# Kernel optimization log

Hardware: AMD Instinct MI355X
Metric: run time of the kernel (lower is better)

Reference implementation:

```python
import jax, jax.numpy as jnp
import numpy as np

N_NODES = 50000
N_EDGES = 800000
IN_DIM = 128
HIDDEN = 64
HEADS = 4
OUT_DIM = 32
NEG_SLOPE = 0.2  # PyG GATConv default negative_slope


def _glorot(key, shape):
    fan = shape[0] + shape[-1]
    return jax.random.normal(key, shape, dtype=jnp.float32) * jnp.sqrt(2.0 / fan)


def setup_inputs() -> dict:
    key = jax.random.key(0)
    ks = jax.random.split(key, 8)
    x = jax.random.normal(ks[0], (N_NODES, IN_DIM), dtype=jnp.float32)
    edge_index = jax.random.randint(ks[1], (2, N_EDGES), 0, N_NODES, dtype=jnp.int64)
    return {
        "x": x,
        "edge_index": edge_index,
        "W1": _glorot(ks[2], (IN_DIM, HEADS * HIDDEN)),
        "a_src1": _glorot(ks[3], (HEADS, HIDDEN)),
        "a_dst1": _glorot(ks[4], (HEADS, HIDDEN)),
        "b1": jnp.zeros((HEADS * HIDDEN,), dtype=jnp.float32),
        "W2": _glorot(ks[5], (HEADS * HIDDEN, OUT_DIM)),
        "a_src2": _glorot(ks[6], (1, OUT_DIM)),
        "a_dst2": _glorot(ks[7], (1, OUT_DIM)),
        "b2": jnp.zeros((OUT_DIM,), dtype=jnp.float32),
    }


def gat_conv(x, src, dst, W, a_src, a_dst, b, heads, feat, concat):
    """PyG-style GATConv (self-loops already appended to src/dst)."""
    n = x.shape[0]
    h = (x @ W).reshape(n, heads, feat)              # [N, H, F]
    alpha_s = jnp.einsum("nhf,hf->nh", h, a_src)     # [N, H]
    alpha_d = jnp.einsum("nhf,hf->nh", h, a_dst)     # [N, H]
    logits = jax.nn.leaky_relu(alpha_s[src] + alpha_d[dst], NEG_SLOPE)  # [E, H]
    # segment softmax over edges grouped by destination node
    seg_max = jax.ops.segment_max(logits, dst, num_segments=n)          # [N, H]
    expd = jnp.exp(logits - seg_max[dst])
    seg_sum = jax.ops.segment_sum(expd, dst, num_segments=n)            # [N, H]
    alpha = expd / (seg_sum[dst] + 1e-16)                               # [E, H]
    # scatter-aggregate weighted messages from source nodes
    out = jax.ops.segment_sum(h[src] * alpha[:, :, None], dst, num_segments=n)  # [N, H, F]
    out = out.reshape(n, heads * feat) if concat else out.mean(axis=1)
    return out + b


def reference(x, edge_index, W1, a_src1, a_dst1, b1, W2, a_src2, a_dst2, b2):
    n = x.shape[0]
    loop = jnp.arange(n, dtype=edge_index.dtype)
    src = jnp.concatenate([edge_index[0], loop])  # add_self_loops=True (PyG default)
    dst = jnp.concatenate([edge_index[1], loop])
    h = jax.nn.elu(gat_conv(x, src, dst, W1, a_src1, a_dst1, b1, HEADS, HIDDEN, True))
    return gat_conv(h, src, dst, W2, a_src2, a_dst2, b2, 1, OUT_DIM, False)
```

## Files before the change

kernel.cpp:

```cpp
#include <hip/hip_runtime.h>
#include <hip/hip_bf16.h>

#define N_NODES 50000
#define N_EDGES 800000
#define E_TOT   850000
#define IN_DIM  128
#define C1      256
#define HEADS   4
#define HID     64
#define OUT_DIM 32
#define NEG_SLOPE 0.2f
#define SCAN_NBLK 196

typedef __attribute__((ext_vector_type(8))) short bf16x8;
typedef __attribute__((ext_vector_type(8))) unsigned short u16x8;
typedef __attribute__((ext_vector_type(4))) float f32x4;

__device__ __forceinline__ void edge_sd(const int* __restrict__ ei, int e, int& s, int& d) {
    if (e < N_EDGES) { s = ei[e]; d = ei[N_EDGES + e]; }
    else             { s = d = e - N_EDGES; }
}

__device__ __forceinline__ unsigned short f2bf(float f) {
    unsigned u = __float_as_uint(f);
    u += 0x7fffu + ((u >> 16) & 1u);
    return (unsigned short)(u >> 16);
}
__device__ __forceinline__ float bf2f(unsigned short u) {
    return __uint_as_float(((unsigned)u) << 16);
}
__device__ __forceinline__ float4 bf4_to_f4(ushort4 v) {
    return make_float4(bf2f(v.x), bf2f(v.y), bf2f(v.z), bf2f(v.w));
}

__global__ __launch_bounds__(256) void setup_kernel(const float* __restrict__ W1,
                                                    const float* __restrict__ W2,
                                                    unsigned short* __restrict__ Bp1,
                                                    unsigned short* __restrict__ Bp2,
                                                    int* __restrict__ degcur) {
    int tid = blockIdx.x * 256 + threadIdx.x;
    if (tid < 2 * N_NODES) degcur[tid] = 0;
    if (tid < IN_DIM * C1) {
        int j = tid & 7, q = (tid >> 3) & 3, n = (tid >> 5) & 255, K0 = tid >> 13;
        int k = K0 * 32 + q * 8 + j;
        Bp1[tid] = f2bf(W1[k * C1 + n]);
        if (tid < C1 * OUT_DIM) {
            int j2 = tid & 7, q2 = (tid >> 3) & 3, n2 = (tid >> 5) & 31, K02 = tid >> 10;
            int k2 = K02 * 32 + q2 * 8 + j2;
            Bp2[tid] = f2bf(W2[k2 * OUT_DIM + n2]);
        }
    }
}

__global__ __launch_bounds__(256) void deg_kernel(const int* __restrict__ ei,
                                                  int* __restrict__ deg) {
    int e = blockIdx.x * 256 + threadIdx.x;
    if (e >= E_TOT) return;
    int s, d; edge_sd(ei, e, s, d);
    atomicAdd(&deg[d], 1);
}

__global__ __launch_bounds__(256) void scanA_kernel(const int* __restrict__ deg,
                                                    int* __restrict__ incl,
                                                    int* __restrict__ blocksum) {
    __shared__ int sm[256];
    int t = threadIdx.x, idx = blockIdx.x * 256 + t;
    int v = (idx < N_NODES) ? deg[idx] : 0;
    sm[t] = v; __syncthreads();
#pragma unroll
    for (int off = 1; off < 256; off <<= 1) {
        int u = (t >= off) ? sm[t - off] : 0;
        __syncthreads();
        sm[t] += u;
        __syncthreads();
    }
    if (idx < N_NODES) incl[idx] = sm[t];
    if (t == 255) blocksum[blockIdx.x] = sm[t];
}

__global__ __launch_bounds__(256) void scanC_kernel(const int* __restrict__ deg,
                                                    const int* __restrict__ incl,
                                                    const int* __restrict__ blocksum,
                                                    int* __restrict__ row_start) {
    __shared__ int wsum[4];
    int t = threadIdx.x;
    int v = (t < (int)blockIdx.x) ? blocksum[t] : 0;
#pragma unroll
    for (int m = 32; m >= 1; m >>= 1) v += __shfl_xor(v, m, 64);
    if ((t & 63) == 0) wsum[t >> 6] = v;
    __syncthreads();
    int off = wsum[0] + wsum[1] + wsum[2] + wsum[3];
    int idx = blockIdx.x * 256 + t;
    if (idx >= N_NODES) return;
    row_start[idx] = off + incl[idx] - deg[idx];
    if (idx == N_NODES - 1) row_start[N_NODES] = off + incl[idx];
}

__global__ __launch_bounds__(256) void scatter_kernel(const int* __restrict__ ei,
                                                      const int* __restrict__ row_start,
                                                      int* __restrict__ cursor,
                                                      int* __restrict__ csr_src) {
    int e = blockIdx.x * 256 + threadIdx.x;
    if (e >= E_TOT) return;
    int s, d; edge_sd(ei, e, s, d);
    int pos = atomicAdd(&cursor[d], 1);
    csr_src[row_start[d] + pos] = s;
}

__global__ __launch_bounds__(256) void gemm1_kernel(const float* __restrict__ x,
                                                    const unsigned short* __restrict__ Bp,
                                                    const float* __restrict__ a_src1,
                                                    const float* __restrict__ a_dst1,
                                                    unsigned short* __restrict__ h1b,
                                                    float* __restrict__ as1,
                                                    float* __restrict__ ad1) {
    __shared__ unsigned short xs[16][136];
    const int t = threadIdx.x;
    const int row0 = blockIdx.x * 16;
    {
        int r = t >> 4, k0 = (t & 15) * 8;
        const float* xp = &x[(size_t)(row0 + r) * IN_DIM + k0];
        float4 v0 = *(const float4*)xp;
        float4 v1 = *(const float4*)(xp + 4);
        ushort4 o0, o1;
        o0.x = f2bf(v0.x); o0.y = f2bf(v0.y); o0.z = f2bf(v0.z); o0.w = f2bf(v0.w);
        o1.x = f2bf(v1.x); o1.y = f2bf(v1.y); o1.z = f2bf(v1.z); o1.w = f2bf(v1.w);
        *(ushort4*)&xs[r][k0] = o0;
        *(ushort4*)&xs[r][k0 + 4] = o1;
    }
    __syncthreads();
    const int wave = t >> 6;
    const int lane = t & 63;
    const int nl = lane & 15, q = lane >> 4;
    f32x4 acc[4];
    f32x4 z = {0.f, 0.f, 0.f, 0.f};
    acc[0] = z; acc[1] = z; acc[2] = z; acc[3] = z;
#pragma unroll
    for (int K0 = 0; K0 < 4; ++K0) {
        bf16x8 af = *(const bf16x8*)&xs[nl][K0 * 32 + q * 8];
#pragma unroll
        for (int sub = 0; sub < 4; ++sub) {
            int n = wave * 64 + sub * 16 + nl;
            bf16x8 bfv = *(const bf16x8*)&Bp[((size_t)(K0 * 256 + n) * 4 + q) * 8];
            acc[sub] = __builtin_amdgcn_mfma_f32_16x16x32_bf16(af, bfv, acc[sub], 0, 0, 0);
        }
    }
    float asv[4], adv[4];
#pragma unroll
    for (int sub = 0; sub < 4; ++sub) {
        asv[sub] = a_src1[wave * 64 + sub * 16 + nl];
        adv[sub] = a_dst1[wave * 64 + sub * 16 + nl];
    }
#pragma unroll
    for (int r = 0; r < 4; ++r) {
        int gr = row0 + q * 4 + r;
        float ps = 0.f, pd = 0.f;
#pragma unroll
        for (int sub = 0; sub < 4; ++sub) {
            float v = acc[sub][r];
            h1b[(size_t)gr * C1 + wave * 64 + sub * 16 + nl] = f2bf(v);
            ps += v * asv[sub];
            pd += v * adv[sub];
        }
#pragma unroll
        for (int m = 8; m >= 1; m >>= 1) {
            ps += __shfl_xor(ps, m, 16);
            pd += __shfl_xor(pd, m, 16);
        }
        if (nl == 0) {
            as1[gr * 4 + wave] = ps;
            ad1[gr * 4 + wave] = pd;
        }
    }
}

__global__ __launch_bounds__(256) void agg1_kernel(const int* __restrict__ csr_src,
                                                   const int* __restrict__ row_start,
                                                   const unsigned short* __restrict__ h1b,
                                                   const float* __restrict__ as1,
                                                   const float* __restrict__ ad1,
                                                   const float* __restrict__ b1,
                                                   unsigned short* __restrict__ hpb) {
    int n = (blockIdx.x * 256 + threadIdx.x) >> 6;
    if (n >= N_NODES) return;
    int lane = threadIdx.x & 63;
    int h = lane >> 4;
    int beg = row_start[n], end = row_start[n + 1];
    float ad = ad1[n * 4 + h];
    float4 acc = make_float4(0.f, 0.f, 0.f, 0.f);
    float sumw = 0.f;
    int i = beg;
    for (; i + 8 <= end; i += 8) {
        int s[8];
#pragma unroll
        for (int u = 0; u < 8; ++u) s[u] = csr_src[i + u];
        ushort4 rv[8];
#pragma unroll
        for (int u = 0; u < 8; ++u) rv[u] = *(const ushort4*)&h1b[(size_t)s[u] * C1 + lane * 4];
        float a[8];
#pragma unroll
        for (int u = 0; u < 8; ++u) a[u] = as1[s[u] * 4 + h];
#pragma unroll
        for (int u = 0; u < 8; ++u) {
            float l = a[u] + ad;
            l = l > 0.f ? l : NEG_SLOPE * l;
            float w = __expf(l);
            sumw += w;
            float4 f = bf4_to_f4(rv[u]);
            acc.x += w * f.x; acc.y += w * f.y; acc.z += w * f.z; acc.w += w * f.w;
        }
    }
    if (i < end) {
        int s[8]; bool va[8];
#pragma unroll
        for (int u = 0; u < 8; ++u) {
            va[u] = (i + u) < end;
            s[u] = csr_src[va[u] ? i + u : beg];
        }
        ushort4 rv[8];
#pragma unroll
        for (int u = 0; u < 8; ++u) rv[u] = *(const ushort4*)&h1b[(size_t)s[u] * C1 + lane * 4];
        float a[8];
#pragma unroll
        for (int u = 0; u < 8; ++u) a[u] = as1[s[u] * 4 + h];
#pragma unroll
        for (int u = 0; u < 8; ++u) {
            float l = a[u] + ad;
            l = l > 0.f ? l : NEG_SLOPE * l;
            float w = va[u] ? __expf(l) : 0.f;
            sumw += w;
            float4 f = bf4_to_f4(rv[u]);
            acc.x += w * f.x; acc.y += w * f.y; acc.z += w * f.z; acc.w += w * f.w;
        }
    }
    float inv = 1.f / (sumw + 1e-16f);
    const float4 bv = *(const float4*)&b1[lane * 4];
    float v0 = acc.x * inv + bv.x;
    float v1 = acc.y * inv + bv.y;
    float v2 = acc.z * inv + bv.z;
    float v3 = acc.w * inv + bv.w;
    v0 = v0 > 0.f ? v0 : __expf(v0) - 1.f;
    v1 = v1 > 0.f ? v1 : __expf(v1) - 1.f;
    v2 = v2 > 0.f ? v2 : __expf(v2) - 1.f;
    v3 = v3 > 0.f ? v3 : __expf(v3) - 1.f;
    ushort4 o;
    o.x = f2bf(v0); o.y = f2bf(v1); o.z = f2bf(v2); o.w = f2bf(v3);
    *(ushort4*)&hpb[(size_t)n * C1 + lane * 4] = o;
}

__global__ __launch_bounds__(256) void gemm2_kernel(const unsigned short* __restrict__ hpb,
                                                    const unsigned short* __restrict__ Bp2,
                                                    const float* __restrict__ a_src2,
                                                    const float* __restrict__ a_dst2,
                                                    unsigned short* __restrict__ h2b,
                                                    float* __restrict__ as2,
                                                    float* __restrict__ ad2) {
    __shared__ unsigned short xs[64][264];
    const int t = threadIdx.x;
    const int row0 = blockIdx.x * 64;
    for (int idx = t; idx < 2048; idx += 256) {
        int r = idx >> 5, ch = (idx & 31) * 8;
        int gr = row0 + r;
        u16x8 v = {0, 0, 0, 0, 0, 0, 0, 0};
        if (gr < N_NODES) v = *(const u16x8*)&hpb[(size_t)gr * C1 + ch];
        *(u16x8*)&xs[r][ch] = v;
    }
    __syncthreads();
    const int wave = t >> 6, lane = t & 63;
    const int nl = lane & 15, q = lane >> 4;
    f32x4 acc0 = {0.f, 0.f, 0.f, 0.f}, acc1 = {0.f, 0.f, 0.f, 0.f};
#pragma unroll
    for (int K0 = 0; K0 < 8; ++K0) {
        bf16x8 af = *(const bf16x8*)&xs[wave * 16 + nl][K0 * 32 + q * 8];
        bf16x8 b0 = *(const bf16x8*)&Bp2[((size_t)(K0 * 32 + nl) * 4 + q) * 8];
        bf16x8 b1v = *(const bf16x8*)&Bp2[((size_t)(K0 * 32 + 16 + nl) * 4 + q) * 8];
        acc0 = __builtin_amdgcn_mfma_f32_16x16x32_bf16(af, b0, acc0, 0, 0, 0);
        acc1 = __builtin_amdgcn_mfma_f32_16x16x32_bf16(af, b1v, acc1, 0, 0, 0);
    }
    float a_s0 = a_src2[nl], a_s1 = a_src2[16 + nl];
    float a_d0 = a_dst2[nl], a_d1 = a_dst2[16 + nl];
#pragma unroll
    for (int r = 0; r < 4; ++r) {
        int gr = row0 + wave * 16 + q * 4 + r;
        if (gr < N_NODES) {
            h2b[(size_t)gr * OUT_DIM + nl] = f2bf(acc0[r]);
            h2b[(size_t)gr * OUT_DIM + 16 + nl] = f2bf(acc1[r]);
            float ps = acc0[r] * a_s0 + acc1[r] * a_s1;
            float pd = acc0[r] * a_d0 + acc1[r] * a_d1;
#pragma unroll
            for (int m = 8; m >= 1; m >>= 1) {
                ps += __shfl_xor(ps, m, 16);
                pd += __shfl_xor(pd, m, 16);
            }
            if (nl == 0) { as2[gr] = ps; ad2[gr] = pd; }
        }
    }
}

__global__ __launch_bounds__(256) void agg2_kernel(const int* __restrict__ csr_src,
                                                   const int* __restrict__ row_start,
                                                   const unsigned short* __restrict__ h2b,
                                                   const float* __restrict__ as2,
                                                   const float* __restrict__ ad2,
                                                   const float* __restrict__ b2,
                                                   float* __restrict__ out) {
    int n = (blockIdx.x * 256 + threadIdx.x) >> 6;
    if (n >= N_NODES) return;
    int lane = threadIdx.x & 63;
    int g  = lane >> 3;
    int c4 = lane & 7;
    int beg = row_start[n], end = row_start[n + 1];
    float ad = ad2[n];
    float4 acc = make_float4(0.f, 0.f, 0.f, 0.f);
    float sumw = 0.f;
    for (int i = beg; i < end; i += 8) {
        int idx = i + g;
        bool valid = idx < end;
        int ic = valid ? idx : beg;
        int s = csr_src[ic];
        float l = as2[s] + ad;
        l = l > 0.f ? l : NEG_SLOPE * l;
        float w = valid ? __expf(l) : 0.f;
        sumw += w;
        float4 hv = bf4_to_f4(*(const ushort4*)&h2b[(size_t)s * OUT_DIM + c4 * 4]);
        acc.x += w * hv.x; acc.y += w * hv.y; acc.z += w * hv.z; acc.w += w * hv.w;
    }
#pragma unroll
    for (int m = 8; m <= 32; m <<= 1) {
        sumw  += __shfl_xor(sumw, m, 64);
        acc.x += __shfl_xor(acc.x, m, 64);
        acc.y += __shfl_xor(acc.y, m, 64);
        acc.z += __shfl_xor(acc.z, m, 64);
        acc.w += __shfl_xor(acc.w, m, 64);
    }
    if (g == 0) {
        float inv = 1.f / (sumw + 1e-16f);
        const float4 bv = *(const float4*)&b2[c4 * 4];
        *(float4*)&out[(size_t)n * OUT_DIM + c4 * 4] =
            make_float4(acc.x * inv + bv.x, acc.y * inv + bv.y,
                        acc.z * inv + bv.z, acc.w * inv + bv.w);
    }
}

extern "C" void kernel_launch(void* const* d_in, const int* in_sizes, int n_in,
                              void* d_out, int out_size, void* d_ws, size_t ws_size,
                              hipStream_t stream) {
    const float* x      = (const float*)d_in[0];
    const int*   ei     = (const int*)d_in[1];
    const float* W1     = (const float*)d_in[2];
    const float* a_src1 = (const float*)d_in[3];
    const float* a_dst1 = (const float*)d_in[4];
    const float* b1     = (const float*)d_in[5];
    const float* W2     = (const float*)d_in[6];
    const float* a_src2 = (const float*)d_in[7];
    const float* a_dst2 = (const float*)d_in[8];
    const float* b2     = (const float*)d_in[9];
    float* out = (float*)d_out;

    unsigned short* h1b = (unsigned short*)d_ws;
    unsigned short* hpb = h1b + 12800000;
    unsigned short* h2b = hpb + 12800000;
    unsigned short* Bp1 = h2b + 1600000;
    unsigned short* Bp2 = Bp1 + 32768;
    float* as1    = (float*)(Bp2 + 8192);
    float* ad1    = as1 + 200000;
    float* as2    = ad1 + 200000;
    float* ad2    = as2 + 50000;
    int* csr_src  = (int*)(ad2 + 50000);
    int* row_start= csr_src + E_TOT;
    int* deg      = row_start + (N_NODES + 1);
    int* cursor   = deg + N_NODES;
    int* incl     = cursor + N_NODES;
    int* blocksum = incl + N_NODES;

    const int EB = (E_TOT + 255) / 256;
    setup_kernel<<<391, 256, 0, stream>>>(W1, W2, Bp1, Bp2, deg);
    deg_kernel<<<EB, 256, 0, stream>>>(ei, deg);
    scanA_kernel<<<SCAN_NBLK, 256, 0, stream>>>(deg, incl, blocksum);
    scanC_kernel<<<SCAN_NBLK, 256, 0, stream>>>(deg, incl, blocksum, row_start);
    scatter_kernel<<<EB, 256, 0, stream>>>(ei, row_start, cursor, csr_src);

    gemm1_kernel<<<N_NODES / 16, 256, 0, stream>>>(x, Bp1, a_src1, a_dst1, h1b, as1, ad1);
    agg1_kernel<<<(N_NODES * 64 + 255) / 256, 256, 0, stream>>>(csr_src, row_start, h1b, as1, ad1, b1, hpb);

    gemm2_kernel<<<(N_NODES + 63) / 64, 256, 0, stream>>>(hpb, Bp2, a_src2, a_dst2, h2b, as2, ad2);
    agg2_kernel<<<(N_NODES * 64 + 255) / 256, 256, 0, stream>>>(csr_src, row_start, h2b, as2, ad2, b2, out);
}
```

Baseline: 302.9 us.

## Record atomic slot in degree pass and precompute CSR-ordered edge weights

The degree kernel now stores each edge's atomic slot, so the scatter pass places edges without a second atomic. Scatter now runs after gemm1 and also computes exp(leaky_relu(as+ad)) for all four heads per edge. It writes these weights in CSR order into a new buffer. agg1 reads the precomputed weights contiguously instead of gathering as1 and recomputing the exp in every lane. Row bounds and source indices are made wave-uniform with readfirstlane. The cost is an extra per-edge weight buffer and position array, roughly 17 MB more memory traffic.

```diff
diff --git a/kernel.cpp b/kernel.cpp
--- a/kernel.cpp
+++ b/kernel.cpp
@@ -37,9 +37,9 @@
                                                     const float* __restrict__ W2,
                                                     unsigned short* __restrict__ Bp1,
                                                     unsigned short* __restrict__ Bp2,
-                                                    int* __restrict__ degcur) {
+                                                    int* __restrict__ deg) {
     int tid = blockIdx.x * 256 + threadIdx.x;
-    if (tid < 2 * N_NODES) degcur[tid] = 0;
+    if (tid < N_NODES) deg[tid] = 0;
     if (tid < IN_DIM * C1) {
         int j = tid & 7, q = (tid >> 3) & 3, n = (tid >> 5) & 255, K0 = tid >> 13;
         int k = K0 * 32 + q * 8 + j;
@@ -53,11 +53,12 @@
 }
 
 __global__ __launch_bounds__(256) void deg_kernel(const int* __restrict__ ei,
-                                                  int* __restrict__ deg) {
+                                                  int* __restrict__ deg,
+                                                  int* __restrict__ pos) {
     int e = blockIdx.x * 256 + threadIdx.x;
     if (e >= E_TOT) return;
     int s, d; edge_sd(ei, e, s, d);
-    atomicAdd(&deg[d], 1);
+    pos[e] = atomicAdd(&deg[d], 1);
 }
 
 __global__ __launch_bounds__(256) void scanA_kernel(const int* __restrict__ deg,
@@ -96,15 +97,27 @@
     if (idx == N_NODES - 1) row_start[N_NODES] = off + incl[idx];
 }
 
-__global__ __launch_bounds__(256) void scatter_kernel(const int* __restrict__ ei,
-                                                      const int* __restrict__ row_start,
-                                                      int* __restrict__ cursor,
-                                                      int* __restrict__ csr_src) {
+__global__ __launch_bounds__(256) void scatter_w_kernel(const int* __restrict__ ei,
+                                                        const int* __restrict__ row_start,
+                                                        const int* __restrict__ pos,
+                                                        const float* __restrict__ as1,
+                                                        const float* __restrict__ ad1,
+                                                        int* __restrict__ csr_src,
+                                                        float* __restrict__ wc) {
     int e = blockIdx.x * 256 + threadIdx.x;
     if (e >= E_TOT) return;
     int s, d; edge_sd(ei, e, s, d);
-    int pos = atomicAdd(&cursor[d], 1);
-    csr_src[row_start[d] + pos] = s;
+    int p = row_start[d] + pos[e];
+    csr_src[p] = s;
+    float4 av = *(const float4*)&as1[s * 4];
+    float4 bv = *(const float4*)&ad1[d * 4];
+    float l0 = av.x + bv.x, l1 = av.y + bv.y, l2 = av.z + bv.z, l3 = av.w + bv.w;
+    l0 = l0 > 0.f ? l0 : NEG_SLOPE * l0;
+    l1 = l1 > 0.f ? l1 : NEG_SLOPE * l1;
+    l2 = l2 > 0.f ? l2 : NEG_SLOPE * l2;
+    l3 = l3 > 0.f ? l3 : NEG_SLOPE * l3;
+    *(float4*)&wc[(size_t)p * 4] =
+        make_float4(__expf(l0), __expf(l1), __expf(l2), __expf(l3));
 }
 
 __global__ __launch_bounds__(256) void gemm1_kernel(const float* __restrict__ x,
@@ -177,60 +190,56 @@
 __global__ __launch_bounds__(256) void agg1_kernel(const int* __restrict__ csr_src,
                                                    const int* __restrict__ row_start,
                                                    const unsigned short* __restrict__ h1b,
-                                                   const float* __restrict__ as1,
-                                                   const float* __restrict__ ad1,
+                                                   const float* __restrict__ wc,
                                                    const float* __restrict__ b1,
                                                    unsigned short* __restrict__ hpb) {
     int n = (blockIdx.x * 256 + threadIdx.x) >> 6;
     if (n >= N_NODES) return;
     int lane = threadIdx.x & 63;
     int h = lane >> 4;
-    int beg = row_start[n], end = row_start[n + 1];
-    float ad = ad1[n * 4 + h];
+    int beg = __builtin_amdgcn_readfirstlane(row_start[n]);
+    int end = __builtin_amdgcn_readfirstlane(row_start[n + 1]);
     float4 acc = make_float4(0.f, 0.f, 0.f, 0.f);
     float sumw = 0.f;
     int i = beg;
     for (; i + 8 <= end; i += 8) {
         int s[8];
 #pragma unroll
-        for (int u = 0; u < 8; ++u) s[u] = csr_src[i + u];
+        for (int u = 0; u < 8; ++u) s[u] = __builtin_amdgcn_readfirstlane(csr_src[i + u]);
+        float w[8];
+#pragma unroll
+        for (int u = 0; u < 8; ++u) w[u] = wc[(size_t)(i + u) * 4 + h];
         ushort4 rv[8];
 #pragma unroll
         for (int u = 0; u < 8; ++u) rv[u] = *(const ushort4*)&h1b[(size_t)s[u] * C1 + lane * 4];
-        float a[8];
-#pragma unroll
-        for (int u = 0; u < 8; ++u) a[u] = as1[s[u] * 4 + h];
 #pragma unroll
         for (int u = 0; u < 8; ++u) {
-            float l = a[u] + ad;
-            l = l > 0.f ? l : NEG_SLOPE * l;
-            float w = __expf(l);
-            sumw += w;
+            sumw += w[u];
             float4 f = bf4_to_f4(rv[u]);
-            acc.x += w * f.x; acc.y += w * f.y; acc.z += w * f.z; acc.w += w * f.w;
+            acc.x += w[u] * f.x; acc.y += w[u] * f.y;
+            acc.z += w[u] * f.z; acc.w += w[u] * f.w;
         }
     }
     if (i < end) {
-        int s[8]; bool va[8];
+        int s[8]; int ic[8]; bool va[8];
 #pragma unroll
         for (int u = 0; u < 8; ++u) {
             va[u] = (i + u) < end;
-            s[u] = csr_src[va[u] ? i + u : beg];
-        }
+            ic[u] = va[u] ? i + u : beg;
+            s[u] = __builtin_amdgcn_readfirstlane(csr_src[ic[u]]);
+        }
+        float w[8];
+#pragma unroll
+        for (int u = 0; u < 8; ++u) w[u] = va[u] ? wc[(size_t)ic[u] * 4 + h] : 0.f;
         ushort4 rv[8];
 #pragma unroll
         for (int u = 0; u < 8; ++u) rv[u] = *(const ushort4*)&h1b[(size_t)s[u] * C1 + lane * 4];
-        float a[8];
-#pragma unroll
-        for (int u = 0; u < 8; ++u) a[u] = as1[s[u] * 4 + h];
 #pragma unroll
         for (int u = 0; u < 8; ++u) {
-            float l = a[u] + ad;
-            l = l > 0.f ? l : NEG_SLOPE * l;
-            float w = va[u] ? __expf(l) : 0.f;
-            sumw += w;
+            sumw += w[u];
             float4 f = bf4_to_f4(rv[u]);
-            acc.x += w * f.x; acc.y += w * f.y; acc.z += w * f.z; acc.w += w * f.w;
+            acc.x += w[u] * f.x; acc.y += w[u] * f.y;
+            acc.z += w[u] * f.z; acc.w += w[u] * f.w;
         }
     }
     float inv = 1.f / (sumw + 1e-16f);
@@ -309,7 +318,8 @@
     int lane = threadIdx.x & 63;
     int g  = lane >> 3;
     int c4 = lane & 7;
-    int beg = row_start[n], end = row_start[n + 1];
+    int beg = __builtin_amdgcn_readfirstlane(row_start[n]);
+    int end = __builtin_amdgcn_readfirstlane(row_start[n + 1]);
     float ad = ad2[n];
     float4 acc = make_float4(0.f, 0.f, 0.f, 0.f);
     float sumw = 0.f;
@@ -366,22 +376,23 @@
     float* ad1    = as1 + 200000;
     float* as2    = ad1 + 200000;
     float* ad2    = as2 + 50000;
-    int* csr_src  = (int*)(ad2 + 50000);
+    float* wc     = ad2 + 50000;
+    int* csr_src  = (int*)(wc + (size_t)E_TOT * 4);
     int* row_start= csr_src + E_TOT;
     int* deg      = row_start + (N_NODES + 1);
-    int* cursor   = deg + N_NODES;
-    int* incl     = cursor + N_NODES;
+    int* pos      = deg + N_NODES;
+    int* incl     = pos + E_TOT;
     int* blocksum = incl + N_NODES;
 
     const int EB = (E_TOT + 255) / 256;
-    setup_kernel<<<391, 256, 0, stream>>>(W1, W2, Bp1, Bp2, deg);
-    deg_kernel<<<EB, 256, 0, stream>>>(ei, deg);
+    setup_kernel<<<SCAN_NBLK, 256, 0, stream>>>(W1, W2, Bp1, Bp2, deg);
+    deg_kernel<<<EB, 256, 0, stream>>>(ei, deg, pos);
     scanA_kernel<<<SCAN_NBLK, 256, 0, stream>>>(deg, incl, blocksum);
     scanC_kernel<<<SCAN_NBLK, 256, 0, stream>>>(deg, incl, blocksum, row_start);
-    scatter_kernel<<<EB, 256, 0, stream>>>(ei, row_start, cursor, csr_src);
 
     gemm1_kernel<<<N_NODES / 16, 256, 0, stream>>>(x, Bp1, a_src1, a_dst1, h1b, as1, ad1);
-    agg1_kernel<<<(N_NODES * 64 + 255) / 256, 256, 0, stream>>>(csr_src, row_start, h1b, as1, ad1, b1, hpb);
+    scatter_w_kernel<<<EB, 256, 0, stream>>>(ei, row_start, pos, as1, ad1, csr_src, wc);
+    agg1_kernel<<<(N_NODES * 64 + 255) / 256, 256, 0, stream>>>(csr_src, row_start, h1b, wc, b1, hpb);
 
     gemm2_kernel<<<(N_NODES + 63) / 64, 256, 0, stream>>>(hpb, Bp2, a_src2, a_dst2, h2b, as2, ad2);
     agg2_kernel<<<(N_NODES * 64 + 255) / 256, 256, 0, stream>>>(csr_src, row_start, h2b, as2, ad2, b2, out);
```

After: 272.9 us. -9.9%, faster.

## Fuse degree counting into gemm1 and simplify CSR build with atomic-offset scan

Applied to the files above, without the earlier changes.

Degree counting moves into the tail of gemm1, and each edge's slot is recorded from the atomicAdd return value. That removes the separate deg kernel and the cursor atomics in scatter. The two-pass scan is replaced by a single pass that takes block bases from an atomic counter, so row order across blocks becomes arbitrary and row ends come from deg. The aggregation kernels use readfirstlane to make indices uniform, unroll deeper (16 edges per step), and use a fmax-based leaky-relu. This cuts launches and atomics but gives up the natural ordering of csr rows.

```diff
diff --git a/kernel.cpp b/kernel.cpp
--- a/kernel.cpp
+++ b/kernel.cpp
@@ -11,6 +11,8 @@
 #define OUT_DIM 32
 #define NEG_SLOPE 0.2f
 #define SCAN_NBLK 196
+#define G1_BLOCKS 3125
+#define EDGES_PER_G1 272
 
 typedef __attribute__((ext_vector_type(8))) short bf16x8;
 typedef __attribute__((ext_vector_type(8))) unsigned short u16x8;
@@ -32,14 +34,17 @@
 __device__ __forceinline__ float4 bf4_to_f4(ushort4 v) {
     return make_float4(bf2f(v.x), bf2f(v.y), bf2f(v.z), bf2f(v.w));
 }
+__device__ __forceinline__ float lrelu_exp(float l) {
+    return __expf(fmaxf(l, NEG_SLOPE * l));
+}
 
 __global__ __launch_bounds__(256) void setup_kernel(const float* __restrict__ W1,
                                                     const float* __restrict__ W2,
                                                     unsigned short* __restrict__ Bp1,
                                                     unsigned short* __restrict__ Bp2,
-                                                    int* __restrict__ degcur) {
+                                                    int* __restrict__ deg) {
     int tid = blockIdx.x * 256 + threadIdx.x;
-    if (tid < 2 * N_NODES) degcur[tid] = 0;
+    if (tid < N_NODES + 1) deg[tid] = 0;
     if (tid < IN_DIM * C1) {
         int j = tid & 7, q = (tid >> 3) & 3, n = (tid >> 5) & 255, K0 = tid >> 13;
         int k = K0 * 32 + q * 8 + j;
@@ -52,68 +57,16 @@
     }
 }
 
-__global__ __launch_bounds__(256) void deg_kernel(const int* __restrict__ ei,
-                                                  int* __restrict__ deg) {
-    int e = blockIdx.x * 256 + threadIdx.x;
-    if (e >= E_TOT) return;
-    int s, d; edge_sd(ei, e, s, d);
-    atomicAdd(&deg[d], 1);
-}
-
-__global__ __launch_bounds__(256) void scanA_kernel(const int* __restrict__ deg,
-                                                    int* __restrict__ incl,
-                                                    int* __restrict__ blocksum) {
-    __shared__ int sm[256];
-    int t = threadIdx.x, idx = blockIdx.x * 256 + t;
-    int v = (idx < N_NODES) ? deg[idx] : 0;
-    sm[t] = v; __syncthreads();
-#pragma unroll
-    for (int off = 1; off < 256; off <<= 1) {
-        int u = (t >= off) ? sm[t - off] : 0;
-        __syncthreads();
-        sm[t] += u;
-        __syncthreads();
-    }
-    if (idx < N_NODES) incl[idx] = sm[t];
-    if (t == 255) blocksum[blockIdx.x] = sm[t];
-}
-
-__global__ __launch_bounds__(256) void scanC_kernel(const int* __restrict__ deg,
-                                                    const int* __restrict__ incl,
-                                                    const int* __restrict__ blocksum,
-                                                    int* __restrict__ row_start) {
-    __shared__ int wsum[4];
-    int t = threadIdx.x;
-    int v = (t < (int)blockIdx.x) ? blocksum[t] : 0;
-#pragma unroll
-    for (int m = 32; m >= 1; m >>= 1) v += __shfl_xor(v, m, 64);
-    if ((t & 63) == 0) wsum[t >> 6] = v;
-    __syncthreads();
-    int off = wsum[0] + wsum[1] + wsum[2] + wsum[3];
-    int idx = blockIdx.x * 256 + t;
-    if (idx >= N_NODES) return;
-    row_start[idx] = off + incl[idx] - deg[idx];
-    if (idx == N_NODES - 1) row_start[N_NODES] = off + incl[idx];
-}
-
-__global__ __launch_bounds__(256) void scatter_kernel(const int* __restrict__ ei,
-                                                      const int* __restrict__ row_start,
-                                                      int* __restrict__ cursor,
-                                                      int* __restrict__ csr_src) {
-    int e = blockIdx.x * 256 + threadIdx.x;
-    if (e >= E_TOT) return;
-    int s, d; edge_sd(ei, e, s, d);
-    int pos = atomicAdd(&cursor[d], 1);
-    csr_src[row_start[d] + pos] = s;
-}
-
 __global__ __launch_bounds__(256) void gemm1_kernel(const float* __restrict__ x,
                                                     const unsigned short* __restrict__ Bp,
                                                     const float* __restrict__ a_src1,
                                                     const float* __restrict__ a_dst1,
+                                                    const int* __restrict__ ei,
                                                     unsigned short* __restrict__ h1b,
                                                     float* __restrict__ as1,
-                                                    float* __restrict__ ad1) {
+                                                    float* __restrict__ ad1,
+                                                    int* __restrict__ deg,
+                                                    int* __restrict__ pos) {
     __shared__ unsigned short xs[16][136];
     const int t = threadIdx.x;
     const int row0 = blockIdx.x * 16;
@@ -172,10 +125,46 @@
             ad1[gr * 4 + wave] = pd;
         }
     }
+    int base = blockIdx.x * EDGES_PER_G1;
+    for (int e = base + t; e < base + EDGES_PER_G1; e += 256) {
+        int s, d; edge_sd(ei, e, s, d);
+        pos[e] = atomicAdd(&deg[d], 1);
+    }
+}
+
+__global__ __launch_bounds__(256) void scan_kernel(const int* __restrict__ deg,
+                                                   int* __restrict__ counter,
+                                                   int* __restrict__ row_start) {
+    __shared__ int sm[256];
+    __shared__ int base;
+    int t = threadIdx.x, idx = blockIdx.x * 256 + t;
+    int v = (idx < N_NODES) ? deg[idx] : 0;
+    sm[t] = v; __syncthreads();
+#pragma unroll
+    for (int off = 1; off < 256; off <<= 1) {
+        int u = (t >= off) ? sm[t - off] : 0;
+        __syncthreads();
+        sm[t] += u;
+        __syncthreads();
+    }
+    if (t == 255) base = atomicAdd(counter, sm[255]);
+    __syncthreads();
+    if (idx < N_NODES) row_start[idx] = base + sm[t] - v;
+}
+
+__global__ __launch_bounds__(256) void scatter_kernel(const int* __restrict__ ei,
+                                                      const int* __restrict__ row_start,
+                                                      const int* __restrict__ pos,
+                                                      int* __restrict__ csr_src) {
+    int e = blockIdx.x * 256 + threadIdx.x;
+    if (e >= E_TOT) return;
+    int s, d; edge_sd(ei, e, s, d);
+    csr_src[row_start[d] + pos[e]] = s;
 }
 
 __global__ __launch_bounds__(256) void agg1_kernel(const int* __restrict__ csr_src,
                                                    const int* __restrict__ row_start,
+                                                   const int* __restrict__ deg,
                                                    const unsigned short* __restrict__ h1b,
                                                    const float* __restrict__ as1,
                                                    const float* __restrict__ ad1,
@@ -185,52 +174,72 @@
     if (n >= N_NODES) return;
     int lane = threadIdx.x & 63;
     int h = lane >> 4;
-    int beg = row_start[n], end = row_start[n + 1];
+    int beg = __builtin_amdgcn_readfirstlane(row_start[n]);
+    int end = beg + __builtin_amdgcn_readfirstlane(deg[n]);
     float ad = ad1[n * 4 + h];
     float4 acc = make_float4(0.f, 0.f, 0.f, 0.f);
     float sumw = 0.f;
     int i = beg;
-    for (; i + 8 <= end; i += 8) {
-        int s[8];
-#pragma unroll
-        for (int u = 0; u < 8; ++u) s[u] = csr_src[i + u];
-        ushort4 rv[8];
-#pragma unroll
-        for (int u = 0; u < 8; ++u) rv[u] = *(const ushort4*)&h1b[(size_t)s[u] * C1 + lane * 4];
-        float a[8];
-#pragma unroll
-        for (int u = 0; u < 8; ++u) a[u] = as1[s[u] * 4 + h];
-#pragma unroll
-        for (int u = 0; u < 8; ++u) {
-            float l = a[u] + ad;
-            l = l > 0.f ? l : NEG_SLOPE * l;
-            float w = __expf(l);
+    for (; i + 16 <= end; i += 16) {
+        int s[16];
+#pragma unroll
+        for (int u = 0; u < 16; ++u) s[u] = __builtin_amdgcn_readfirstlane(csr_src[i + u]);
+        float a[16];
+#pragma unroll
+        for (int u = 0; u < 16; ++u) a[u] = as1[s[u] * 4 + h];
+        ushort4 rv[16];
+#pragma unroll
+        for (int u = 0; u < 16; ++u) rv[u] = *(const ushort4*)&h1b[(size_t)s[u] * C1 + lane * 4];
+#pragma unroll
+        for (int u = 0; u < 16; ++u) {
+            float w = lrelu_exp(a[u] + ad);
             sumw += w;
             float4 f = bf4_to_f4(rv[u]);
-            acc.x += w * f.x; acc.y += w * f.y; acc.z += w * f.z; acc.w += w * f.w;
-        }
-    }
-    if (i < end) {
-        int s[8]; bool va[8];
+            acc.x += w * f.x; acc.y += w * f.y;
+            acc.z += w * f.z; acc.w += w * f.w;
+        }
+    }
+    if (i + 8 <= end) {
+        int s[8];
+#pragma unroll
+        for (int u = 0; u < 8; ++u) s[u] = __builtin_amdgcn_readfirstlane(csr_src[i + u]);
+        float a[8];
+#pragma unroll
+        for (int u = 0; u < 8; ++u) a[u] = as1[s[u] * 4 + h];
+        ushort4 rv[8];
+#pragma unroll
+        for (int u = 0; u < 8; ++u) rv[u] = *(const ushort4*)&h1b[(size_t)s[u] * C1 + lane * 4];
 #pragma unroll
         for (int u = 0; u < 8; ++u) {
-            va[u] = (i + u) < end;
-            s[u] = csr_src[va[u] ? i + u : beg];
-        }
-        ushort4 rv[8];
-#pragma unroll
-        for (int u = 0; u < 8; ++u) rv[u] = *(const ushort4*)&h1b[(size_t)s[u] * C1 + lane * 4];
-        float a[8];
-#pragma unroll
-        for (int u = 0; u < 8; ++u) a[u] = as1[s[u] * 4 + h];
-#pragma unroll
-        for (int u = 0; u < 8; ++u) {
-            float l = a[u] + ad;
-            l = l > 0.f ? l : NEG_SLOPE * l;
-            float w = va[u] ? __expf(l) : 0.f;
+            float w = lrelu_exp(a[u] + ad);
             sumw += w;
             float4 f = bf4_to_f4(rv[u]);
-            acc.x += w * f.x; acc.y += w * f.y; acc.z += w * f.z; acc.w += w * f.w;
+            acc.x += w * f.x; acc.y += w * f.y;
+            acc.z += w * f.z; acc.w += w * f.w;
+        }
+        i += 8;
+    }
+    if (i < end) {
+        int s[8]; float va[8];
+#pragma unroll
+        for (int u = 0; u < 8; ++u) {
+            bool v = (i + u) < end;
+            va[u] = v ? 1.f : 0.f;
+            s[u] = __builtin_amdgcn_readfirstlane(csr_src[v ? i + u : beg]);
+        }
+        float a[8];
+#pragma unroll
+        for (int u = 0; u < 8; ++u) a[u] = as1[s[u] * 4 + h];
+        ushort4 rv[8];
+#pragma unroll
+        for (int u = 0; u < 8; ++u) rv[u] = *(const ushort4*)&h1b[(size_t)s[u] * C1 + lane * 4];
+#pragma unroll
+        for (int u = 0; u < 8; ++u) {
+            float w = va[u] * lrelu_exp(a[u] + ad);
+            sumw += w;
+            float4 f = bf4_to_f4(rv[u]);
+            acc.x += w * f.x; acc.y += w * f.y;
+            acc.z += w * f.z; acc.w += w * f.w;
         }
     }
     float inv = 1.f / (sumw + 1e-16f);
@@ -299,6 +308,7 @@
 
 __global__ __launch_bounds__(256) void agg2_kernel(const int* __restrict__ csr_src,
                                                    const int* __restrict__ row_start,
+                                                   const int* __restrict__ deg,
                                                    const unsigned short* __restrict__ h2b,
                                                    const float* __restrict__ as2,
                                                    const float* __restrict__ ad2,
@@ -309,21 +319,23 @@
     int lane = threadIdx.x & 63;
     int g  = lane >> 3;
     int c4 = lane & 7;
-    int beg = row_start[n], end = row_start[n + 1];
+    int beg = __builtin_amdgcn_readfirstlane(row_start[n]);
+    int end = beg + __builtin_amdgcn_readfirstlane(deg[n]);
     float ad = ad2[n];
     float4 acc = make_float4(0.f, 0.f, 0.f, 0.f);
     float sumw = 0.f;
-    for (int i = beg; i < end; i += 8) {
-        int idx = i + g;
-        bool valid = idx < end;
-        int ic = valid ? idx : beg;
-        int s = csr_src[ic];
-        float l = as2[s] + ad;
-        l = l > 0.f ? l : NEG_SLOPE * l;
-        float w = valid ? __expf(l) : 0.f;
-        sumw += w;
-        float4 hv = bf4_to_f4(*(const ushort4*)&h2b[(size_t)s * OUT_DIM + c4 * 4]);
-        acc.x += w * hv.x; acc.y += w * hv.y; acc.z += w * hv.z; acc.w += w * hv.w;
+    for (int i = beg; i < end; i += 16) {
+#pragma unroll
+        for (int b = 0; b < 2; ++b) {
+            int idx = i + b * 8 + g;
+            bool valid = idx < end;
+            int ic = valid ? idx : beg;
+            int s = csr_src[ic];
+            float w = valid ? lrelu_exp(as2[s] + ad) : 0.f;
+            sumw += w;
+            float4 hv = bf4_to_f4(*(const ushort4*)&h2b[(size_t)s * OUT_DIM + c4 * 4]);
+            acc.x += w * hv.x; acc.y += w * hv.y; acc.z += w * hv.z; acc.w += w * hv.w;
+        }
     }
 #pragma unroll
     for (int m = 8; m <= 32; m <<= 1) {
@@ -368,21 +380,17 @@
     float* ad2    = as2 + 50000;
     int* csr_src  = (int*)(ad2 + 50000);
     int* row_start= csr_src + E_TOT;
-    int* deg      = row_start + (N_NODES + 1);
-    int* cursor   = deg + N_NODES;
-    int* incl     = cursor + N_NODES;
-    int* blocksum = incl + N_NODES;
-
-    const int EB = (E_TOT + 255) / 256;
-    setup_kernel<<<391, 256, 0, stream>>>(W1, W2, Bp1, Bp2, deg);
-    deg_kernel<<<EB, 256, 0, stream>>>(ei, deg);
-    scanA_kernel<<<SCAN_NBLK, 256, 0, stream>>>(deg, incl, blocksum);
-    scanC_kernel<<<SCAN_NBLK, 256, 0, stream>>>(deg, incl, blocksum, row_start);
-    scatter_kernel<<<EB, 256, 0, stream>>>(ei, row_start, cursor, csr_src);
-
-    gemm1_kernel<<<N_NODES / 16, 256, 0, stream>>>(x, Bp1, a_src1, a_dst1, h1b, as1, ad1);
-    agg1_kernel<<<(N_NODES * 64 + 255) / 256, 256, 0, stream>>>(csr_src, row_start, h1b, as1, ad1, b1, hpb);
-
+    int* deg      = row_start + N_NODES;
+    int* pos      = deg + N_NODES + 1;
+
+    setup_kernel<<<SCAN_NBLK, 256, 0, stream>>>(W1, W2, Bp1, Bp2, deg);
+    gemm1_kernel<<<G1_BLOCKS, 256, 0, stream>>>(x, Bp1, a_src1, a_dst1, ei,
+                                                h1b, as1, ad1, deg, pos);
+    scan_kernel<<<SCAN_NBLK, 256, 0, stream>>>(deg, deg + N_NODES, row_start);
+    scatter_kernel<<<(E_TOT + 255) / 256, 256, 0, stream>>>(ei, row_start, pos, csr_src);
+    agg1_kernel<<<(N_NODES * 64 + 255) / 256, 256, 0, stream>>>(csr_src, row_start, deg,
+                                                                h1b, as1, ad1, b1, hpb);
     gemm2_kernel<<<(N_NODES + 63) / 64, 256, 0, stream>>>(hpb, Bp2, a_src2, a_dst2, h2b, as2, ad2);
-    agg2_kernel<<<(N_NODES * 64 + 255) / 256, 256, 0, stream>>>(csr_src, row_start, h2b, as2, ad2, b2, out);
-}
+    agg2_kernel<<<(N_NODES * 64 + 255) / 256, 256, 0, stream>>>(csr_src, row_start, deg,
+                                                                h2b, as2, ad2, b2, out);
+}
```

New measurement: 250.7 us, median of 2. 1.21x faster.
